# Performance work log

Hardware: AMD Instinct MI355X
Metric: run time of the kernel (lower is better)

The kernel has to match this reference:

```python
import jax, jax.numpy as jnp
import numpy as np

B, WAYS, SHOTS, C, H, W = 64, 10, 5, 128, 32, 32


def setup_inputs() -> dict:
    key = jax.random.key(0)
    k1, k2, k3 = jax.random.split(key, 3)
    q = jax.random.normal(k1, (B, C, H, W), dtype=jnp.float32)
    support = jax.random.normal(k2, (WAYS, SHOTS, C, H, W), dtype=jnp.float32)
    conv_w = jax.random.normal(k3, (H * W,), dtype=jnp.float32) * 0.03
    return {"q": q, "support": support, "conv_w": conv_w}


def reference(q, support, conv_w):
    b, c, h, w = q.shape
    ways, shots = support.shape[:2]
    hw = h * w
    # --- cal_covariance: per-class channel covariance ---
    # [ways, shots, C, h, w] -> [ways, C, shots*h*w]
    s = support.transpose(0, 2, 1, 3, 4).reshape(ways, c, shots * hw)
    s = s - s.mean(axis=2, keepdims=True)
    denom = jnp.float32(shots * hw - 1)
    cov = jnp.einsum('jcn,jdn->jcd', s, s) / denom  # [ways, C, C]
    # --- cal_similarity: per-pixel quadratic form diag(Q^T Sigma Q) ---
    qf = q.reshape(b, c, hw)
    qn = qf / jnp.linalg.norm(qf, axis=2, keepdims=True)  # L2 norm per channel row
    t = jnp.einsum('jcd,bdp->bjcp', cov, qn)              # [B, ways, C, hw]
    sim = jnp.einsum('bcp,bjcp->bjp', qn, t)              # diagonal only: [B, ways, hw]
    # --- classifier1: LeakyReLU(0.2) -> Dropout (eval identity) -> Conv1d(1,1,k=hw,stride=hw,bias=False) ---
    x = sim.reshape(b, ways * hw)
    x = jnp.where(x >= 0, x, 0.2 * x)
    out = jnp.einsum('bjp,p->bj', x.reshape(b, ways, hw), conv_w)  # [B, ways]
    return out
```

## Files before the change

### kernel.cpp

```cpp
#include <hip/hip_runtime.h>

typedef unsigned short u16;
typedef unsigned int u32;
typedef __attribute__((ext_vector_type(8))) short bf16x8;
typedef __attribute__((ext_vector_type(4))) short bf16x4v;
typedef __attribute__((ext_vector_type(4))) float f32x4;

#define NWAYS 10
#define NC 128
#define NHW 1024

__device__ __forceinline__ u16 f2bf(float f) {
  u32 u = __builtin_bit_cast(u32, f);
  return (u16)((u + 0x7fffu + ((u >> 16) & 1u)) >> 16);
}
__device__ __forceinline__ float bf2f(u16 h) {
  u32 u = ((u32)h) << 16;
  return __builtin_bit_cast(float, u);
}

__global__ __launch_bounds__(512) void k_phase1(const float* __restrict__ sup,
                                                const float* __restrict__ q,
                                                const float* __restrict__ cw,
                                                u16* __restrict__ Gpartb,
                                                float* __restrict__ mpart,
                                                u16* __restrict__ Wrawb,
                                                float* __restrict__ ss,
                                                float* __restrict__ out) {
  __shared__ u16 smem[NC * 256];
  __shared__ float saux[NC];
  int bid = blockIdx.x;
  int t = threadIdx.x;
  int w = t >> 6, l = t & 63, lr = l & 15, lg = l >> 4;

  if (bid < 100) {
    int j = bid / 10, cid = bid % 10;
    int shot = cid >> 1, p0 = (cid & 1) * 512;
    const float* base = sup + ((size_t)(j * 5 + shot) * NC) * NHW + p0;
    u16* traw = smem;

    float4 v[8];
    auto load_chunk = [&](int chunk) {
#pragma unroll
      for (int it = 0; it < 8; ++it) {
        int idx = it * 512 + t;
        int c = idx >> 5, pos = idx & 31;
        v[it] = *(const float4*)(base + (size_t)c * NHW + chunk * 128 + pos * 4);
      }
    };
    auto store_chunk = [&](int chunk) {
      (void)chunk;
#pragma unroll
      for (int it = 0; it < 8; ++it) {
        int idx = it * 512 + t;
        int c = idx >> 5, pos = idx & 31;
        float4 vv = v[it];
        int nl = pos * 4;
        int off = c * 128 + (((nl >> 3) ^ (c & 15)) << 3) + (nl & 7);
        bf16x4v hr;
        hr[0] = (short)f2bf(vv.x); hr[1] = (short)f2bf(vv.y);
        hr[2] = (short)f2bf(vv.z); hr[3] = (short)f2bf(vv.w);
        *(bf16x4v*)&traw[off] = hr;
        float s = vv.x + vv.y + vv.z + vv.w;
#pragma unroll
        for (int m = 1; m <= 16; m <<= 1) s += __shfl_xor(s, m, 64);
        if ((l & 31) == 0) saux[c] += s;
      }
    };

    load_chunk(0);
    if (t < NC) saux[t] = 0.f;
    __syncthreads();
    store_chunk(0);
    __syncthreads();

    f32x4 acc[8];
#pragma unroll
    for (int bt = 0; bt < 8; ++bt) acc[bt] = (f32x4){0.f, 0.f, 0.f, 0.f};
#pragma unroll 1
    for (int chunk = 0; chunk < 4; ++chunk) {
      if (chunk < 3) load_chunk(chunk + 1);
#pragma unroll
      for (int kb = 0; kb < 4; ++kb) {
        int nn = kb * 32 + lg * 8;
        int arow = w * 16 + lr;
        bf16x8 fa = *(const bf16x8*)&traw[arow * 128 + (((nn >> 3) ^ (arow & 15)) << 3)];
        bf16x8 fb[8];
#pragma unroll
        for (int bt = 0; bt < 8; ++bt) {
          int drow = bt * 16 + lr;
          fb[bt] = *(const bf16x8*)&traw[drow * 128 + (((nn >> 3) ^ (drow & 15)) << 3)];
        }
#pragma unroll
        for (int bt = 0; bt < 8; ++bt)
          acc[bt] = __builtin_amdgcn_mfma_f32_16x16x32_bf16(fa, fb[bt], acc[bt], 0, 0, 0);
      }
      __syncthreads();
      if (chunk < 3) { store_chunk(chunk + 1); __syncthreads(); }
    }

    if (t < NC) mpart[(size_t)bid * NC + t] = saux[t];
    u16* gp = Gpartb + ((size_t)bid << 14);
#pragma unroll
    for (int bt = 0; bt < 8; ++bt)
#pragma unroll
      for (int r = 0; r < 4; ++r) {
        int cr = w * 16 + lg * 4 + r;
        int d = bt * 16 + lr;
        gp[cr * NC + d] = f2bf(acc[bt][r]);
      }
  } else {
    int bid2 = bid - 100;
    if (bid2 < 2) {
      int o = bid2 * 512 + t;
      if (o < 64 * NWAYS) out[o] = 0.f;
    }
    int b = bid2 >> 1, half = bid2 & 1;
    u16* traw = smem;
    u16* twgt = smem + 16384;
    const float* base = q + (size_t)b * NC * NHW + half * 512;
    const float* cwb = cw + half * 512;

    float4 v[8];
    auto load_chunk = [&](int chunk) {
#pragma unroll
      for (int it = 0; it < 8; ++it) {
        int idx = it * 512 + t;
        int c = idx >> 5, pos = idx & 31;
        v[it] = *(const float4*)(base + (size_t)c * NHW + chunk * 128 + pos * 4);
      }
    };
    auto store_chunk = [&](int chunk) {
#pragma unroll
      for (int it = 0; it < 8; ++it) {
        int idx = it * 512 + t;
        int c = idx >> 5, pos = idx & 31;
        float4 vv = v[it];
        float4 wv = *(const float4*)(cwb + chunk * 128 + pos * 4);
        int nl = pos * 4;
        int off = c * 128 + (((nl >> 3) ^ (c & 15)) << 3) + (nl & 7);
        bf16x4v hr, hw;
        hr[0] = (short)f2bf(vv.x); hr[1] = (short)f2bf(vv.y);
        hr[2] = (short)f2bf(vv.z); hr[3] = (short)f2bf(vv.w);
        hw[0] = (short)f2bf(vv.x * wv.x); hw[1] = (short)f2bf(vv.y * wv.y);
        hw[2] = (short)f2bf(vv.z * wv.z); hw[3] = (short)f2bf(vv.w * wv.w);
        *(bf16x4v*)&traw[off] = hr;
        *(bf16x4v*)&twgt[off] = hw;
        float s = vv.x * vv.x + vv.y * vv.y + vv.z * vv.z + vv.w * vv.w;
#pragma unroll
        for (int m = 1; m <= 16; m <<= 1) s += __shfl_xor(s, m, 64);
        if ((l & 31) == 0) saux[c] += s;
      }
    };

    load_chunk(0);
    if (t < NC) saux[t] = 0.f;
    __syncthreads();
    store_chunk(0);
    __syncthreads();

    f32x4 acc[8];
#pragma unroll
    for (int bt = 0; bt < 8; ++bt) acc[bt] = (f32x4){0.f, 0.f, 0.f, 0.f};
#pragma unroll 1
    for (int chunk = 0; chunk < 4; ++chunk) {
      if (chunk < 3) load_chunk(chunk + 1);
#pragma unroll
      for (int kb = 0; kb < 4; ++kb) {
        int nn = kb * 32 + lg * 8;
        int arow = w * 16 + lr;
        bf16x8 fa = *(const bf16x8*)&twgt[arow * 128 + (((nn >> 3) ^ (arow & 15)) << 3)];
        bf16x8 fb[8];
#pragma unroll
        for (int bt = 0; bt < 8; ++bt) {
          int drow = bt * 16 + lr;
          fb[bt] = *(const bf16x8*)&traw[drow * 128 + (((nn >> 3) ^ (drow & 15)) << 3)];
        }
#pragma unroll
        for (int bt = 0; bt < 8; ++bt)
          acc[bt] = __builtin_amdgcn_mfma_f32_16x16x32_bf16(fa, fb[bt], acc[bt], 0, 0, 0);
      }
      __syncthreads();
      if (chunk < 3) { store_chunk(chunk + 1); __syncthreads(); }
    }

    if (t < NC) ss[(size_t)(half * 64 + b) * NC + t] = saux[t];
    u16* wb = Wrawb + ((size_t)(half * 64 + b) << 14);
#pragma unroll
    for (int bt = 0; bt < 8; ++bt)
#pragma unroll
      for (int r = 0; r < 4; ++r) {
        int cr = w * 16 + lg * 4 + r;
        int d = bt * 16 + lr;
        wb[cr * NC + d] = f2bf(acc[bt][r]);
      }
  }
}

__global__ __launch_bounds__(256) void k_fin(const u16* __restrict__ Gpartb,
                                             const float* __restrict__ mpart,
                                             u16* __restrict__ covb) {
  __shared__ float msd[NC];
  int j = blockIdx.x >> 4, rg = blockIdx.x & 15;
  int t = threadIdx.x;
  if (t < NC) {
    float s = 0.f;
#pragma unroll
    for (int k = 0; k < 10; ++k) s += mpart[(size_t)(j * 10 + k) * NC + t];
    msd[t] = s;
  }
  __syncthreads();
  int e = rg * 1024 + t * 4;
  int c = e >> 7, d0 = e & 127;
  float g[4] = {0.f, 0.f, 0.f, 0.f};
#pragma unroll
  for (int k = 0; k < 10; ++k) {
    bf16x4v v = *(const bf16x4v*)(Gpartb + (((size_t)(j * 10 + k)) << 14) + e);
#pragma unroll
    for (int r = 0; r < 4; ++r) g[r] += bf2f((u16)v[r]);
  }
  bf16x4v o;
#pragma unroll
  for (int r = 0; r < 4; ++r)
    o[r] = (short)f2bf((g[r] - msd[c] * msd[d0 + r] * (1.0f / 5120.0f)) * (1.0f / 5119.0f));
  *(bf16x4v*)(covb + (((size_t)j) << 14) + e) = o;
}

__global__ __launch_bounds__(256) void k_wndot(const u16* __restrict__ Wrawb,
                                               const float* __restrict__ ss,
                                               const u16* __restrict__ covb,
                                               float* __restrict__ out) {
  __shared__ float rnl[NC];
  __shared__ float red[4 * NWAYS];
  int b = blockIdx.x >> 2, rg = blockIdx.x & 3;
  int t = threadIdx.x;
  int w = t >> 6, l = t & 63;
  if (t < NC) {
    float s = ss[(size_t)b * NC + t] + ss[(size_t)(64 + b) * NC + t];
    rnl[t] = rsqrtf(s);
  }
  __syncthreads();
  int e = rg * 4096 + t * 16;
  int c = e >> 7, d0 = e & 127;
  float wn[16];
#pragma unroll
  for (int k = 0; k < 16; ++k) wn[k] = 0.f;
#pragma unroll
  for (int qr = 0; qr < 2; ++qr) {
    const u16* src = Wrawb + (((size_t)(qr * 64 + b)) << 14) + e;
    bf16x8 v0 = *(const bf16x8*)src;
    bf16x8 v1 = *(const bf16x8*)(src + 8);
#pragma unroll
    for (int k = 0; k < 8; ++k) { wn[k] += bf2f((u16)v0[k]); wn[8 + k] += bf2f((u16)v1[k]); }
  }
  float rc = rnl[c];
#pragma unroll
  for (int k = 0; k < 16; ++k) wn[k] *= rc * rnl[d0 + k];

  float acc[NWAYS];
#pragma unroll
  for (int j = 0; j < NWAYS; ++j) {
    const u16* cj = covb + ((size_t)j << 14) + e;
    bf16x8 c0 = *(const bf16x8*)cj;
    bf16x8 c1 = *(const bf16x8*)(cj + 8);
    float s = 0.f;
#pragma unroll
    for (int k = 0; k < 8; ++k) s += wn[k] * bf2f((u16)c0[k]) + wn[8 + k] * bf2f((u16)c1[k]);
    acc[j] = s;
  }
#pragma unroll
  for (int j = 0; j < NWAYS; ++j)
#pragma unroll
    for (int m = 1; m <= 32; m <<= 1) acc[j] += __shfl_xor(acc[j], m, 64);
  if (l == 0)
#pragma unroll
    for (int j = 0; j < NWAYS; ++j) red[w * NWAYS + j] = acc[j];
  __syncthreads();
  if (t < NWAYS)
    atomicAdd(&out[b * NWAYS + t],
              red[t] + red[NWAYS + t] + red[2 * NWAYS + t] + red[3 * NWAYS + t]);
}

extern "C" void kernel_launch(void* const* d_in, const int* in_sizes, int n_in,
                              void* d_out, int out_size, void* d_ws, size_t ws_size,
                              hipStream_t stream) {
  (void)in_sizes; (void)n_in; (void)out_size; (void)ws_size;
  const float* q = (const float*)d_in[0];
  const float* sup = (const float*)d_in[1];
  const float* cw = (const float*)d_in[2];
  float* out = (float*)d_out;

  char* p = (char*)d_ws;
  u16* Gpartb = (u16*)p;    p += (size_t)100 * 16384 * 2;
  float* mpart = (float*)p; p += (size_t)100 * 128 * 4;
  u16* covb = (u16*)p;      p += (size_t)10 * 16384 * 2;
  u16* Wrawb = (u16*)p;     p += (size_t)128 * 16384 * 2;
  float* ssb = (float*)p;

  k_phase1<<<228, 512, 0, stream>>>(sup, q, cw, Gpartb, mpart, Wrawb, ssb, out);
  k_fin<<<160, 256, 0, stream>>>(Gpartb, mpart, covb);
  k_wndot<<<256, 256, 0, stream>>>(Wrawb, ssb, covb, out);
}
```

Before: 30.02 us.

## Fuse covariance finalization into quadratic-form kernel via LDS-resident covariance slab

Merges the covariance-finalization kernel into the weighted dot kernel. Each block rebuilds a 32-row slab of all ten class covariances in shared memory from the bf16 partial Gram sums, then reuses that slab for four query images. This removes one launch and the global round-trip of the bf16 covariance. The cost is redundant rebuilding: each slab is recomputed by 16 blocks, which multiplies Gpartb reads, and only 64 blocks run, lowering parallelism.

Result: slower. 45.60 us (+51.9%).

```diff
diff --git a/kernel.cpp b/kernel.cpp
--- a/kernel.cpp
+++ b/kernel.cpp
@@ -197,88 +197,95 @@
   }
 }
 
-__global__ __launch_bounds__(256) void k_fin(const u16* __restrict__ Gpartb,
-                                             const float* __restrict__ mpart,
-                                             u16* __restrict__ covb) {
-  __shared__ float msd[NC];
-  int j = blockIdx.x >> 4, rg = blockIdx.x & 15;
-  int t = threadIdx.x;
-  if (t < NC) {
-    float s = 0.f;
-#pragma unroll
-    for (int k = 0; k < 10; ++k) s += mpart[(size_t)(j * 10 + k) * NC + t];
-    msd[t] = s;
-  }
-  __syncthreads();
-  int e = rg * 1024 + t * 4;
-  int c = e >> 7, d0 = e & 127;
-  float g[4] = {0.f, 0.f, 0.f, 0.f};
-#pragma unroll
-  for (int k = 0; k < 10; ++k) {
-    bf16x4v v = *(const bf16x4v*)(Gpartb + (((size_t)(j * 10 + k)) << 14) + e);
-#pragma unroll
-    for (int r = 0; r < 4; ++r) g[r] += bf2f((u16)v[r]);
-  }
-  bf16x4v o;
-#pragma unroll
-  for (int r = 0; r < 4; ++r)
-    o[r] = (short)f2bf((g[r] - msd[c] * msd[d0 + r] * (1.0f / 5120.0f)) * (1.0f / 5119.0f));
-  *(bf16x4v*)(covb + (((size_t)j) << 14) + e) = o;
-}
-
-__global__ __launch_bounds__(256) void k_wndot(const u16* __restrict__ Wrawb,
-                                               const float* __restrict__ ss,
-                                               const u16* __restrict__ covb,
-                                               float* __restrict__ out) {
-  __shared__ float rnl[NC];
-  __shared__ float red[4 * NWAYS];
-  int b = blockIdx.x >> 2, rg = blockIdx.x & 3;
+__global__ __launch_bounds__(512) void k_wndot2(const u16* __restrict__ Gpartb,
+                                                const float* __restrict__ mpart,
+                                                const u16* __restrict__ Wrawb,
+                                                const float* __restrict__ ss,
+                                                float* __restrict__ out) {
+  __shared__ u16 covs[NWAYS * 32 * NC];
+  __shared__ float msd[NWAYS * NC];
+  __shared__ float rnl[4 * NC];
+  __shared__ float red[8 * NWAYS];
+  int bid = blockIdx.x;
+  int rg = bid >> 4, bg = bid & 15;
   int t = threadIdx.x;
   int w = t >> 6, l = t & 63;
-  if (t < NC) {
-    float s = ss[(size_t)b * NC + t] + ss[(size_t)(64 + b) * NC + t];
-    rnl[t] = rsqrtf(s);
+
+  for (int idx = t; idx < NWAYS * NC; idx += 512) {
+    int j = idx >> 7, c = idx & 127;
+    float s = 0.f;
+#pragma unroll
+    for (int k = 0; k < 10; ++k) s += mpart[(size_t)(j * 10 + k) * NC + c];
+    msd[idx] = s;
+  }
+  {
+    int bb = t >> 7, c = t & 127;
+    int b = bg * 4 + bb;
+    rnl[t] = rsqrtf(ss[(size_t)b * NC + c] + ss[(size_t)(64 + b) * NC + c]);
   }
   __syncthreads();
-  int e = rg * 4096 + t * 16;
-  int c = e >> 7, d0 = e & 127;
-  float wn[16];
-#pragma unroll
-  for (int k = 0; k < 16; ++k) wn[k] = 0.f;
-#pragma unroll
-  for (int qr = 0; qr < 2; ++qr) {
-    const u16* src = Wrawb + (((size_t)(qr * 64 + b)) << 14) + e;
-    bf16x8 v0 = *(const bf16x8*)src;
-    bf16x8 v1 = *(const bf16x8*)(src + 8);
-#pragma unroll
-    for (int k = 0; k < 8; ++k) { wn[k] += bf2f((u16)v0[k]); wn[8 + k] += bf2f((u16)v1[k]); }
-  }
-  float rc = rnl[c];
-#pragma unroll
-  for (int k = 0; k < 16; ++k) wn[k] *= rc * rnl[d0 + k];
-
-  float acc[NWAYS];
-#pragma unroll
-  for (int j = 0; j < NWAYS; ++j) {
-    const u16* cj = covb + ((size_t)j << 14) + e;
-    bf16x8 c0 = *(const bf16x8*)cj;
-    bf16x8 c1 = *(const bf16x8*)(cj + 8);
-    float s = 0.f;
-#pragma unroll
-    for (int k = 0; k < 8; ++k) s += wn[k] * bf2f((u16)c0[k]) + wn[8 + k] * bf2f((u16)c1[k]);
-    acc[j] = s;
-  }
-#pragma unroll
-  for (int j = 0; j < NWAYS; ++j)
-#pragma unroll
-    for (int m = 1; m <= 32; m <<= 1) acc[j] += __shfl_xor(acc[j], m, 64);
-  if (l == 0)
-#pragma unroll
-    for (int j = 0; j < NWAYS; ++j) red[w * NWAYS + j] = acc[j];
+
+#pragma unroll 1
+  for (int i = 0; i < 20; ++i) {
+    int gpos = i * 2048 + t * 4;
+    int j = gpos >> 12, r = (gpos & 4095) >> 7, d0 = gpos & 127;
+    int c = rg * 32 + r;
+    float g[4] = {0.f, 0.f, 0.f, 0.f};
+#pragma unroll
+    for (int k = 0; k < 10; ++k) {
+      bf16x4v v = *(const bf16x4v*)(Gpartb + (((size_t)(j * 10 + k)) << 14) + c * NC + d0);
+#pragma unroll
+      for (int e = 0; e < 4; ++e) g[e] += bf2f((u16)v[e]);
+    }
+    float mc = msd[j * NC + c];
+    bf16x4v o;
+#pragma unroll
+    for (int e = 0; e < 4; ++e)
+      o[e] = (short)f2bf((g[e] - mc * msd[j * NC + d0 + e] * (1.0f / 5120.0f)) * (1.0f / 5119.0f));
+    *(bf16x4v*)&covs[gpos] = o;
+  }
   __syncthreads();
-  if (t < NWAYS)
-    atomicAdd(&out[b * NWAYS + t],
-              red[t] + red[NWAYS + t] + red[2 * NWAYS + t] + red[3 * NWAYS + t]);
+
+#pragma unroll 1
+  for (int bb = 0; bb < 4; ++bb) {
+    int b = bg * 4 + bb;
+    int epos = t * 8;
+    int r = epos >> 7, d0 = epos & 127;
+    int c = rg * 32 + r;
+    float wn[8];
+    {
+      bf16x8 w0 = *(const bf16x8*)(Wrawb + ((size_t)b << 14) + c * NC + d0);
+      bf16x8 w1 = *(const bf16x8*)(Wrawb + ((size_t)(64 + b) << 14) + c * NC + d0);
+      float rc = rnl[bb * NC + c];
+#pragma unroll
+      for (int e = 0; e < 8; ++e)
+        wn[e] = (bf2f((u16)w0[e]) + bf2f((u16)w1[e])) * rc * rnl[bb * NC + d0 + e];
+    }
+    float acc[NWAYS];
+#pragma unroll
+    for (int j = 0; j < NWAYS; ++j) {
+      bf16x8 cv = *(const bf16x8*)&covs[j * 4096 + epos];
+      float s = 0.f;
+#pragma unroll
+      for (int e = 0; e < 8; ++e) s += wn[e] * bf2f((u16)cv[e]);
+      acc[j] = s;
+    }
+#pragma unroll
+    for (int j = 0; j < NWAYS; ++j)
+#pragma unroll
+      for (int m = 1; m <= 32; m <<= 1) acc[j] += __shfl_xor(acc[j], m, 64);
+    if (l == 0)
+#pragma unroll
+      for (int j = 0; j < NWAYS; ++j) red[w * NWAYS + j] = acc[j];
+    __syncthreads();
+    if (t < NWAYS) {
+      float s = 0.f;
+#pragma unroll
+      for (int wv = 0; wv < 8; ++wv) s += red[wv * NWAYS + t];
+      atomicAdd(&out[b * NWAYS + t], s);
+    }
+    __syncthreads();
+  }
 }
 
 extern "C" void kernel_launch(void* const* d_in, const int* in_sizes, int n_in,
@@ -293,11 +300,9 @@
   char* p = (char*)d_ws;
   u16* Gpartb = (u16*)p;    p += (size_t)100 * 16384 * 2;
   float* mpart = (float*)p; p += (size_t)100 * 128 * 4;
-  u16* covb = (u16*)p;      p += (size_t)10 * 16384 * 2;
   u16* Wrawb = (u16*)p;     p += (size_t)128 * 16384 * 2;
   float* ssb = (float*)p;
 
   k_phase1<<<228, 512, 0, stream>>>(sup, q, cw, Gpartb, mpart, Wrawb, ssb, out);
-  k_fin<<<160, 256, 0, stream>>>(Gpartb, mpart, covb);
-  k_wndot<<<256, 256, 0, stream>>>(Wrawb, ssb, covb, out);
-}
+  k_wndot2<<<64, 512, 0, stream>>>(Gpartb, mpart, Wrawb, ssb, out);
+}
```
